# Kernel tuning notes

Measured on AMD Instinct MI355X. Metric: run time of the kernel, lower is better.

## Reference

```python
import jax, jax.numpy as jnp
import numpy as np

N_NODES = 10000
N_EDGES = 320000
N_GRAPHS = 64
L = 3  # num_layers


def _gru(a, h, wih, whh, bih, bhh):
    # torch.nn.GRUCell math: input a, hidden h
    gi = a @ wih.T + bih
    gh = h @ whh.T + bhh
    ir, iz, inn = jnp.split(gi, 3, axis=-1)
    hr, hz, hn = jnp.split(gh, 3, axis=-1)
    r = jax.nn.sigmoid(ir + hr)
    z = jax.nn.sigmoid(iz + hz)
    n = jnp.tanh(inn + r * hn)
    return (1.0 - z) * n + z * h


def _ggc(x, src, dst, w, wih, whh, bih, bhh):
    # PyG GatedGraphConv: pad features up to out_channels, then L rounds of
    # (linear -> scatter-add over edges -> GRUCell update)
    out_ch = w.shape[-1]
    if x.shape[-1] < out_ch:
        x = jnp.concatenate(
            [x, jnp.zeros((x.shape[0], out_ch - x.shape[-1]), x.dtype)], axis=-1)
    for i in range(w.shape[0]):
        m = x @ w[i]                                        # [N, C]
        a = jax.ops.segment_sum(m[src], dst, num_segments=N_NODES)  # scatter-add
        x = _gru(a, x, wih, whh, bih, bhh)
    return x


def setup_inputs() -> dict:
    key = jax.random.key(0)
    ks = jax.random.split(key, 16)
    d1, d2 = 128, 256
    s1, s2 = 1.0 / np.sqrt(d1), 1.0 / np.sqrt(d2)
    x = jax.random.normal(ks[0], (N_NODES, d1), dtype=jnp.float32)
    edge_index = jax.random.randint(ks[1], (2, N_EDGES), 0, N_NODES, dtype=jnp.int64)
    batch = jnp.sort(jax.random.randint(ks[2], (N_NODES,), 0, N_GRAPHS, dtype=jnp.int64))
    return {
        "x": x,
        "edge_index": edge_index,
        "batch": batch,
        "w1": jax.random.normal(ks[3], (L, d1, d1), jnp.float32) * s1,
        "gru1_wih": jax.random.normal(ks[4], (3 * d1, d1), jnp.float32) * s1,
        "gru1_whh": jax.random.normal(ks[5], (3 * d1, d1), jnp.float32) * s1,
        "gru1_bih": jax.random.normal(ks[6], (3 * d1,), jnp.float32) * s1,
        "gru1_bhh": jax.random.normal(ks[7], (3 * d1,), jnp.float32) * s1,
        "w2": jax.random.normal(ks[8], (L, d2, d2), jnp.float32) * s2,
        "gru2_wih": jax.random.normal(ks[9], (3 * d2, d2), jnp.float32) * s2,
        "gru2_whh": jax.random.normal(ks[10], (3 * d2, d2), jnp.float32) * s2,
        "gru2_bih": jax.random.normal(ks[11], (3 * d2,), jnp.float32) * s2,
        "gru2_bhh": jax.random.normal(ks[12], (3 * d2,), jnp.float32) * s2,
        "fc_w": jax.random.normal(ks[13], (6, d2), jnp.float32) * s2,
        "fc_b": jnp.zeros((6,), jnp.float32),
    }


def reference(x, edge_index, batch, w1, gru1_wih, gru1_whh, gru1_bih, gru1_bhh,
              w2, gru2_wih, gru2_whh, gru2_bih, gru2_bhh, fc_w, fc_b):
    src, dst = edge_index[0], edge_index[1]
    y = jax.nn.relu(_ggc(x, src, dst, w1, gru1_wih, gru1_whh, gru1_bih, gru1_bhh))
    y = _ggc(y, src, dst, w2, gru2_wih, gru2_whh, gru2_bih, gru2_bhh)
    y = jax.ops.segment_max(y, batch, num_segments=N_GRAPHS)  # global max pool [G, 256]
    return y @ fc_w.T + fc_b  # [G, 6]
```

## Files before the change

kernel.cpp:

```cpp
#include <hip/hip_runtime.h>

#define NN 10000
#define NNP 10112
#define NE 320000
#define NG 64
#define D1 128
#define D2 256
#define MT128 79

typedef unsigned short u16;
typedef short v8s __attribute__((ext_vector_type(8)));
typedef float v4f __attribute__((ext_vector_type(4)));

__device__ __forceinline__ u16 f2bf(float x) {
    unsigned u = __float_as_uint(x);
    return (u16)((u + 0x7fffu + ((u >> 16) & 1u)) >> 16);
}
__device__ __forceinline__ float bf2f(u16 b) {
    return __uint_as_float(((unsigned)b) << 16);
}
__device__ __forceinline__ float sigm(float x) { return 1.f / (1.f + __expf(-x)); }
__device__ __forceinline__ float tanh_f(float x) {
    float cx = fminf(fmaxf(x, -15.f), 15.f);
    float e = __expf(2.f * cx);
    return (e - 1.f) / (e + 1.f);
}

#define MF(d, a, b) d = __builtin_amdgcn_mfma_f32_16x16x32_bf16(a, b, d, 0, 0, 0)

#define GLDS16(gp, lp)                                                         \
    __builtin_amdgcn_global_load_lds(                                          \
        (__attribute__((address_space(1))) unsigned int*)(unsigned long long)(gp), \
        (__attribute__((address_space(3))) unsigned int*)(lp), 16, 0, 0)


template<int C, int MODE, int OS, int NPT>
__global__ __launch_bounds__(256, 3)
void giqru_k(const u16* __restrict__ Ah, const u16* __restrict__ Al,
             const u16* __restrict__ Xh, const u16* __restrict__ Xl,
             const u16* __restrict__ WcH, const u16* __restrict__ WcL,
             const float* __restrict__ bih, const float* __restrict__ bhh,
             u16* __restrict__ xh_out, u16* __restrict__ xl_out,
             float* __restrict__ xf_out,
             const int* __restrict__ batch, unsigned* __restrict__ pool) {
    const int bid = blockIdx.x;
    const int l_ = bid >> 3;
    const int byt = (bid & 7) * 10 + l_ % 10;
    const int px = l_ / 10;
    if (byt >= MT128) return;
    __shared__ u16 lds[16384];
    const int tid = threadIdx.x;
    const int wave = tid >> 6, lane = tid & 63;
    const int wr = wave >> 1, wc = wave & 1;
    const int quad = lane >> 4, r16 = lane & 15;
    const int bm = byt * 128;
    constexpr int K2 = 2 * C;
    constexpr int NK = K2 >> 5;
    constexpr int CCH = C >> 3;
    const size_t art = (size_t)(byt * 2);
    const size_t wrow = (size_t)px * (K2 >> 3);

    v4f acc[4][4] = {};
    u16 hsh[4][4], hsl[4][4];
    for (int ks = 0; ks < NK; ++ks) {
        const int k0 = ks << 5;
        const bool ap = k0 < C;
        const u16* sh = ap ? Ah : Xh;
        const u16* sl = ap ? Al : Xl;
        const int kc = (ap ? k0 : k0 - C) >> 3;
#pragma unroll
        for (int s2 = 0; s2 < 8; ++s2) {
            int u = s2 * 4 + wave;
            const u16* gp; int ld;
            if (u < 8)       { int t = u >> 2, q = u & 3;
                gp = sh + ((art + t) * CCH + kc + q) * 512;            ld = q * 1024 + t * 512; }
            else if (u < 16) { int v = u - 8; int t = v >> 2, q = v & 3;
                gp = sl + ((art + t) * CCH + kc + q) * 512;            ld = 4096 + q * 1024 + t * 512; }
            else if (u < 24) { int v = u - 16; int q = v >> 1, h = v & 1;
                gp = WcH + (wrow + (k0 >> 3) + q) * 1024 + h * 512;    ld = 8192 + q * 1024 + h * 512; }
            else             { int v = u - 24; int q = v >> 1, h = v & 1;
                gp = WcL + (wrow + (k0 >> 3) + q) * 1024 + h * 512;    ld = 12288 + q * 1024 + h * 512; }
            GLDS16(gp + lane * 8, &lds[ld]);
        }
        __syncthreads();
        if (!ap && (k0 - C) == px * 32) {
            const int kl = wc * 16 + r16;
            const int q = kl >> 3, kr = kl & 7;
#pragma unroll
            for (int i = 0; i < 4; ++i)
#pragma unroll
                for (int r = 0; r < 4; ++r) {
                    int lr = wr * 64 + i * 16 + quad * 4 + r;
                    int idx = q * 1024 + (lr >> 6) * 512 + (lr & 63) * 8 + kr;
                    hsh[i][r] = lds[idx];
                    hsl[i][r] = lds[4096 + idx];
                }
        }
        v8s fah[4], fal[4];
#pragma unroll
        for (int i = 0; i < 4; ++i) {
            int ra = (quad * 128 + wr * 64 + i * 16 + r16) * 8;
            fah[i] = *(const v8s*)&lds[ra];
            fal[i] = *(const v8s*)&lds[4096 + ra];
        }
        const int g2 = ap ? 2 : 3;
        const int p0 = 8192 + (quad * 128 + wc * 64 + r16) * 8;
        v8s w0h = *(const v8s*)&lds[p0];
        v8s w0l = *(const v8s*)&lds[4096 + p0];
        v8s w1h = *(const v8s*)&lds[p0 + 128];
        v8s w1l = *(const v8s*)&lds[4096 + p0 + 128];
        v8s w2h = *(const v8s*)&lds[p0 + g2 * 128];
        v8s w2l = *(const v8s*)&lds[4096 + p0 + g2 * 128];
#pragma unroll
        for (int i = 0; i < 4; ++i) {
            MF(acc[i][0], fah[i], w0h); MF(acc[i][0], fah[i], w0l); MF(acc[i][0], fal[i], w0h);
            MF(acc[i][1], fah[i], w1h); MF(acc[i][1], fah[i], w1l); MF(acc[i][1], fal[i], w1h);
            if (ap) {
                MF(acc[i][2], fah[i], w2h); MF(acc[i][2], fah[i], w2l); MF(acc[i][2], fal[i], w2h);
            } else {
                MF(acc[i][3], fah[i], w2h); MF(acc[i][3], fah[i], w2l); MF(acc[i][3], fal[i], w2h);
            }
        }
        __syncthreads();
    }

    const int c = px * 32 + wc * 16 + r16;
    const float br = bih[c] + bhh[c];
    const float bz = bih[C + c] + bhh[C + c];
    const float bi_n = bih[2 * C + c];
    const float bh_n = bhh[2 * C + c];
    const int cch = c >> 3, cr = c & 7;
#pragma unroll
    for (int i = 0; i < 4; ++i) {
        int R0 = bm + wr * 64 + i * 16 + quad * 4;
#pragma unroll
        for (int r = 0; r < 4; ++r) {
            int R = R0 + r;
            if (R >= NN) continue;
            float rr = sigm(acc[i][0][r] + br);
            float zz = sigm(acc[i][1][r] + bz);
            float nn_ = tanh_f(acc[i][2][r] + bi_n + rr * (acc[i][3][r] + bh_n));
            float h = bf2f(hsh[i][r]) + bf2f(hsl[i][r]);
            float o = (1.f - zz) * nn_ + zz * h;
            if (MODE == 2) {
                unsigned b = __float_as_uint(o);
                unsigned u = (b & 0x80000000u) ? ~b : (b | 0x80000000u);
                atomicMax(&pool[batch[R] * 256 + c], u);
            } else {
                if (MODE == 1) o = fmaxf(o, 0.f);
                size_t ox = ((size_t)(R >> 6) * (OS >> 3) + cch) * 512 + ((R & 63) << 3) + cr;
                u16 hh = f2bf(o);
                xh_out[ox] = hh;
                xl_out[ox] = f2bf(o - bf2f(hh));
                xf_out[(size_t)R * OS + c] = o;
            }
        }
    }
}

__global__ void count_k(const int* __restrict__ dst, int* __restrict__ cnt) {
    int e = blockIdx.x * blockDim.x + threadIdx.x;
    if (e < NE) atomicAdd(&cnt[dst[e]], 1);
}

__global__ void scan_k(const int* __restrict__ cnt, int* __restrict__ off,
                       int* __restrict__ cur) {
    __shared__ int ps[1024];
    const int tid = threadIdx.x;
    const int CH = (NN + 1023) / 1024;
    const int base = tid * CH;
    int s = 0;
    for (int i = 0; i < CH; ++i) {
        int idx = base + i;
        if (idx < NN) s += cnt[idx];
    }
    ps[tid] = s;
    __syncthreads();
    for (int d = 1; d < 1024; d <<= 1) {
        int v = (tid >= d) ? ps[tid - d] : 0;
        __syncthreads();
        ps[tid] += v;
        __syncthreads();
    }
    int run = (tid > 0) ? ps[tid - 1] : 0;
    for (int i = 0; i < CH; ++i) {
        int idx = base + i;
        if (idx <= NN) { off[idx] = run; if (idx < NN) cur[idx] = run; }
        if (idx < NN) run += cnt[idx];
    }
}

__global__ void fill_k(const int* __restrict__ src, const int* __restrict__ dst,
                       int* __restrict__ cur, int* __restrict__ elist) {
    int e = blockIdx.x * blockDim.x + threadIdx.x;
    if (e >= NE) return;
    int p = atomicAdd(&cur[dst[e]], 1);
    elist[p] = src[e];
}

template<int C>
__global__ void gather_k(const float* __restrict__ xf, const int* __restrict__ off,
                         const int* __restrict__ elist,
                         u16* __restrict__ ah, u16* __restrict__ al) {
    constexpr int LPN = C / 4;
    const int GB = gridDim.x;
    const int q = GB >> 3, r = GB & 7;
    const int xx = blockIdx.x & 7, oo = blockIdx.x >> 3;
    const int wg = (xx < r ? xx * (q + 1) : r * (q + 1) + (xx - r) * q) + oo;
    int t = wg * 256 + threadIdx.x;
    int node = t / LPN;
    if (node >= NN) return;
    int c = (t % LPN) * 4;
    int s0 = off[node], s1 = off[node + 1];
    v4f a0 = 0.f, a1 = 0.f, a2 = 0.f, a3 = 0.f;
    int i = s0;
    for (; i + 4 <= s1; i += 4) {
        int e0 = elist[i], e1 = elist[i + 1], e2 = elist[i + 2], e3 = elist[i + 3];
        v4f v0 = *(const v4f*)(xf + (size_t)e0 * C + c);
        v4f v1 = *(const v4f*)(xf + (size_t)e1 * C + c);
        v4f v2 = *(const v4f*)(xf + (size_t)e2 * C + c);
        v4f v3 = *(const v4f*)(xf + (size_t)e3 * C + c);
        a0 += v0; a1 += v1; a2 += v2; a3 += v3;
    }
    for (; i < s1; ++i) {
        int e = elist[i];
        a0 += *(const v4f*)(xf + (size_t)e * C + c);
    }
    v4f acc = (a0 + a1) + (a2 + a3);
    ushort4 h, l;
    h.x = f2bf(acc[0]); l.x = f2bf(acc[0] - bf2f(h.x));
    h.y = f2bf(acc[1]); l.y = f2bf(acc[1] - bf2f(h.y));
    h.z = f2bf(acc[2]); l.z = f2bf(acc[2] - bf2f(h.z));
    h.w = f2bf(acc[3]); l.w = f2bf(acc[3] - bf2f(h.w));
    size_t ox = ((size_t)(node >> 6) * (C >> 3) + (c >> 3)) * 512 + ((node & 63) << 3) + (c & 7);
    *(ushort4*)(ah + ox) = h;
    *(ushort4*)(al + ox) = l;
}

__global__ void weff_k(const float* __restrict__ w, const float* __restrict__ wih,
                       u16* __restrict__ WcH, u16* __restrict__ WcL, int C) {
    __shared__ float As[64 * 65];
    __shared__ float Bs[64 * 65];
    const int k0 = blockIdx.x * 64, jp0 = blockIdx.y * 64, it = blockIdx.z;
    const int tid = threadIdx.x;
    const int tx = tid & 15, ty = tid >> 4;
    const int K2 = 2 * C;
    float acc[4][4] = {};
    for (int j0 = 0; j0 < C; j0 += 64) {
        for (int idx = tid; idx < 4096; idx += 256) {
            int row = idx >> 6, j = idx & 63;
            As[row * 65 + j] = w[((size_t)it * C + k0 + row) * C + j0 + j];
            int jp = jp0 + row;
            int cc = ((jp >> 6) << 4) | (jp & 15);
            int g = (jp >> 4) & 3;
            Bs[row * 65 + j] = (g < 3) ? wih[((size_t)g * C + cc) * C + j0 + j] : 0.f;
        }
        __syncthreads();
        for (int j = 0; j < 64; ++j) {
            float a0 = As[(tx * 4 + 0) * 65 + j];
            float a1 = As[(tx * 4 + 1) * 65 + j];
            float a2 = As[(tx * 4 + 2) * 65 + j];
            float a3 = As[(tx * 4 + 3) * 65 + j];
            float b0 = Bs[(ty * 4 + 0) * 65 + j];
            float b1 = Bs[(ty * 4 + 1) * 65 + j];
            float b2 = Bs[(ty * 4 + 2) * 65 + j];
            float b3 = Bs[(ty * 4 + 3) * 65 + j];
            acc[0][0] += b0 * a0; acc[0][1] += b0 * a1; acc[0][2] += b0 * a2; acc[0][3] += b0 * a3;
            acc[1][0] += b1 * a0; acc[1][1] += b1 * a1; acc[1][2] += b1 * a2; acc[1][3] += b1 * a3;
            acc[2][0] += b2 * a0; acc[2][1] += b2 * a1; acc[2][2] += b2 * a2; acc[2][3] += b2 * a3;
            acc[3][0] += b3 * a0; acc[3][1] += b3 * a1; acc[3][2] += b3 * a2; acc[3][3] += b3 * a3;
        }
        __syncthreads();
    }
    const size_t its = (size_t)it * 8 * C * C;
#pragma unroll
    for (int a = 0; a < 4; ++a) {
        int jp = jp0 + ty * 4 + a;
#pragma unroll
        for (int b = 0; b < 4; ++b) {
            int k = k0 + tx * 4 + b;
            float v = acc[a][b];
            u16 h = f2bf(v);
            size_t o = its + ((size_t)(jp >> 7) * (K2 >> 3) + (k >> 3)) * 1024 + ((jp & 127) << 3) + (k & 7);
            WcH[o] = h;
            WcL[o] = f2bf(v - bf2f(h));
        }
    }
}

__global__ void prep_k(const float* __restrict__ whh1, const float* __restrict__ whh2,
                       const float* __restrict__ xin,
                       u16* __restrict__ Wc1h, u16* __restrict__ Wc1l,
                       u16* __restrict__ Wc2h, u16* __restrict__ Wc2l,
                       u16* __restrict__ xh, u16* __restrict__ xl) {
    const int q1 = 3 * 512 * 128;
    const int q2 = 3 * 1024 * 256;
    int t = blockIdx.x * blockDim.x + threadIdx.x;
    if (t < q1) {
        int it = t / (512 * 128), r = t - it * (512 * 128);
        int jp = r >> 7, kk = r & 127;
        int c = ((jp >> 6) << 4) | (jp & 15);
        int g = (jp >> 4) & 3;
        float v = (g == 0) ? whh1[c * D1 + kk]
                : (g == 1) ? whh1[(D1 + c) * D1 + kk]
                : (g == 2) ? 0.f
                           : whh1[(2 * D1 + c) * D1 + kk];
        int k = D1 + kk;
        u16 h = f2bf(v);
        size_t o = (size_t)it * 131072 + ((size_t)(jp >> 7) * 32 + (k >> 3)) * 1024 + ((jp & 127) << 3) + (k & 7);
        Wc1h[o] = h; Wc1l[o] = f2bf(v - bf2f(h)); return;
    }
    t -= q1;
    if (t < q2) {
        int it = t / (1024 * 256), r = t - it * (1024 * 256);
        int jp = r >> 8, kk = r & 255;
        int c = ((jp >> 6) << 4) | (jp & 15);
        int g = (jp >> 4) & 3;
        float v = (g == 0) ? whh2[c * D2 + kk]
                : (g == 1) ? whh2[(D2 + c) * D2 + kk]
                : (g == 2) ? 0.f
                           : whh2[(2 * D2 + c) * D2 + kk];
        int k = D2 + kk;
        u16 h = f2bf(v);
        size_t o = (size_t)it * 524288 + ((size_t)(jp >> 7) * 64 + (k >> 3)) * 1024 + ((jp & 127) << 3) + (k & 7);
        Wc2h[o] = h; Wc2l[o] = f2bf(v - bf2f(h)); return;
    }
    t -= q2;
    if (t < NN * D1) {
        int n = t >> 7, cc = t & 127;
        float v = xin[t];
        u16 h = f2bf(v);
        size_t o = ((size_t)(n >> 6) * 16 + (cc >> 3)) * 512 + ((n & 63) << 3) + (cc & 7);
        xh[o] = h;
        xl[o] = f2bf(v - bf2f(h));
    }
}

__global__ void pad_k(u16* __restrict__ xh, u16* __restrict__ xl,
                      float* __restrict__ xf) {
    int t = blockIdx.x * blockDim.x + threadIdx.x;
    if (t >= NNP * 128) return;
    int n = t >> 7, c = 128 + (t & 127);
    size_t o = ((size_t)(n >> 6) * 32 + (c >> 3)) * 512 + ((n & 63) << 3) + (c & 7);
    xh[o] = 0;
    xl[o] = 0;
    xf[(size_t)n * 256 + c] = 0.f;
}

__global__ void pool_init_k(unsigned* __restrict__ pool) {
    int t = blockIdx.x * blockDim.x + threadIdx.x;
    if (t < NG * D2) pool[t] = 0x007FFFFFu;
}

__global__ void fc_k(const unsigned* __restrict__ pool, const float* __restrict__ w,
                     const float* __restrict__ b, float* __restrict__ out) {
    int t = blockIdx.x * blockDim.x + threadIdx.x;
    if (t >= NG * 6) return;
    int g = t / 6, o = t - g * 6;
    float s = b[o];
    for (int c = 0; c < D2; ++c) {
        unsigned u = pool[g * D2 + c];
        unsigned bits = (u & 0x80000000u) ? (u ^ 0x80000000u) : ~u;
        s += __uint_as_float(bits) * w[o * D2 + c];
    }
    out[t] = s;
}

extern "C" void kernel_launch(void* const* d_in, const int* in_sizes, int n_in,
                              void* d_out, int out_size, void* d_ws, size_t ws_size,
                              hipStream_t stream) {
    const float* x_in = (const float*)d_in[0];
    const int* ei = (const int*)d_in[1];
    const int* src = ei;
    const int* dst = ei + NE;
    const int* batch = (const int*)d_in[2];
    const float* w1   = (const float*)d_in[3];
    const float* wih1 = (const float*)d_in[4];
    const float* whh1 = (const float*)d_in[5];
    const float* bih1 = (const float*)d_in[6];
    const float* bhh1 = (const float*)d_in[7];
    const float* w2   = (const float*)d_in[8];
    const float* wih2 = (const float*)d_in[9];
    const float* whh2 = (const float*)d_in[10];
    const float* bih2 = (const float*)d_in[11];
    const float* bhh2 = (const float*)d_in[12];
    const float* fcw  = (const float*)d_in[13];
    const float* fcb  = (const float*)d_in[14];
    float* out = (float*)d_out;

    u16* a_h  = (u16*)d_ws;
    u16* a_l  = a_h + (size_t)NNP * 256;
    u16* xA0h = a_l + (size_t)NNP * 256;
    u16* xA0l = xA0h + (size_t)NNP * 128;
    u16* xA1h = xA0l + (size_t)NNP * 128;
    u16* xA1l = xA1h + (size_t)NNP * 128;
    u16* xB0h = xA1l + (size_t)NNP * 128;
    u16* xB0l = xB0h + (size_t)NNP * 256;
    u16* xB1h = xB0l + (size_t)NNP * 256;
    u16* xB1l = xB1h + (size_t)NNP * 256;
    u16* Wc1h = xB1l + (size_t)NNP * 256;
    u16* Wc1l = Wc1h + (size_t)3 * 512 * 256;
    u16* Wc2h = Wc1l + (size_t)3 * 512 * 256;
    u16* Wc2l = Wc2h + (size_t)3 * 1024 * 512;
    float* xfA = (float*)(Wc2l + (size_t)3 * 1024 * 512);
    float* xfB = xfA + (size_t)NNP * 128;
    int* cnt   = (int*)(xfB + (size_t)NNP * 256);
    int* off   = cnt + NN;
    int* cur   = off + NN + 1;
    int* elist = cur + NN;
    unsigned* pool = (unsigned*)(elist + NE);

    hipMemsetAsync(cnt, 0, NN * sizeof(int), stream);
    count_k<<<(NE + 255) / 256, 256, 0, stream>>>(dst, cnt);
    scan_k<<<1, 1024, 0, stream>>>(cnt, off, cur);
    fill_k<<<(NE + 255) / 256, 256, 0, stream>>>(src, dst, cur, elist);
    {
        int total = 3 * 512 * 128 + 3 * 1024 * 256 + NN * D1;
        prep_k<<<(total + 255) / 256, 256, 0, stream>>>(
            whh1, whh2, x_in, Wc1h, Wc1l, Wc2h, Wc2l, xA0h, xA0l);
    }
    weff_k<<<dim3(D1 / 64, 4 * D1 / 64, 3), 256, 0, stream>>>(w1, wih1, Wc1h, Wc1l, D1);
    weff_k<<<dim3(D2 / 64, 4 * D2 / 64, 3), 256, 0, stream>>>(w2, wih2, Wc2h, Wc2l, D2);
    pad_k<<<(NNP * 128 + 255) / 256, 256, 0, stream>>>(xB0h, xB0l, xfB);
    pool_init_k<<<(NG * D2 + 255) / 256, 256, 0, stream>>>(pool);

    const int G1 = 8 * 10 * 4;
    const int G2 = 8 * 10 * 8;
    const int GG1 = (NN * (D1 / 4) + 255) / 256;
    const int GG2 = (NN * (D2 / 4) + 255) / 256;
    const size_t W1S = 131072, W2S = 524288;

    gather_k<D1><<<GG1, 256, 0, stream>>>(x_in, off, elist, a_h, a_l);
    giqru_k<D1, 0, 128, 4><<<G1, 256, 0, stream>>>(
        a_h, a_l, xA0h, xA0l, Wc1h, Wc1l, bih1, bhh1,
        xA1h, xA1l, xfA, nullptr, nullptr);

    gather_k<D1><<<GG1, 256, 0, stream>>>(xfA, off, elist, a_h, a_l);
    giqru_k<D1, 0, 128, 4><<<G1, 256, 0, stream>>>(
        a_h, a_l, xA1h, xA1l, Wc1h + W1S, Wc1l + W1S, bih1, bhh1,
        xA0h, xA0l, xfA, nullptr, nullptr);

    gather_k<D1><<<GG1, 256, 0, stream>>>(xfA, off, elist, a_h, a_l);
    giqru_k<D1, 1, 256, 4><<<G1, 256, 0, stream>>>(
        a_h, a_l, xA0h, xA0l, Wc1h + 2 * W1S, Wc1l + 2 * W1S, bih1, bhh1,
        xB0h, xB0l, xfB, nullptr, nullptr);

    gather_k<D2><<<GG2, 256, 0, stream>>>(xfB, off, elist, a_h, a_l);
    giqru_k<D2, 0, 256, 8><<<G2, 256, 0, stream>>>(
        a_h, a_l, xB0h, xB0l, Wc2h, Wc2l, bih2, bhh2,
        xB1h, xB1l, xfB, nullptr, nullptr);

    gather_k<D2><<<GG2, 256, 0, stream>>>(xfB, off, elist, a_h, a_l);
    giqru_k<D2, 0, 256, 8><<<G2, 256, 0, stream>>>(
        a_h, a_l, xB1h, xB1l, Wc2h + W2S, Wc2l + W2S, bih2, bhh2,
        xB0h, xB0l, xfB, nullptr, nullptr);

    gather_k<D2><<<GG2, 256, 0, stream>>>(xfB, off, elist, a_h, a_l);
    giqru_k<D2, 2, 256, 8><<<G2, 256, 0, stream>>>(
        a_h, a_l, xB0h, xB0l, Wc2h + 2 * W2S, Wc2l + 2 * W2S, bih2, bhh2,
        nullptr, nullptr, nullptr, batch, pool);

    fc_k<<<1, 512, 0, stream>>>(pool, fcw, fcb, out);
}
```

Baseline: 583.5 us.

## Partition edge gather by source-node chunk to improve cache locality

Edges are bucketed by destination node and by one of four source-node ranges, and each gather becomes four passes, one per source range. Partial sums accumulate in an fp32 buffer, and the last pass converts them to the split-bf16 tiled layout. Each pass touches a smaller slice of the feature table so gathers should hit in L2 more often. The cost is four launches per gather, extra read/write traffic for partial sums, and shorter per-pass edge loops with less memory parallelism.

```diff
diff --git a/kernel.cpp b/kernel.cpp
--- a/kernel.cpp
+++ b/kernel.cpp
@@ -7,6 +7,8 @@
 #define D1 128
 #define D2 256
 #define MT128 79
+#define NCH 4
+#define CHS 2500
 
 typedef unsigned short u16;
 typedef short v8s __attribute__((ext_vector_type(8)));
@@ -158,21 +160,23 @@
     }
 }
 
-__global__ void count_k(const int* __restrict__ dst, int* __restrict__ cnt) {
+__global__ void count_k(const int* __restrict__ src, const int* __restrict__ dst,
+                        int* __restrict__ cnt) {
     int e = blockIdx.x * blockDim.x + threadIdx.x;
-    if (e < NE) atomicAdd(&cnt[dst[e]], 1);
+    if (e < NE) atomicAdd(&cnt[dst[e] * NCH + src[e] / CHS], 1);
 }
 
 __global__ void scan_k(const int* __restrict__ cnt, int* __restrict__ off,
                        int* __restrict__ cur) {
     __shared__ int ps[1024];
     const int tid = threadIdx.x;
-    const int CH = (NN + 1023) / 1024;
+    const int TOT = NN * NCH;
+    const int CH = (TOT + 1023) / 1024;
     const int base = tid * CH;
     int s = 0;
     for (int i = 0; i < CH; ++i) {
         int idx = base + i;
-        if (idx < NN) s += cnt[idx];
+        if (idx < TOT) s += cnt[idx];
     }
     ps[tid] = s;
     __syncthreads();
@@ -185,8 +189,8 @@
     int run = (tid > 0) ? ps[tid - 1] : 0;
     for (int i = 0; i < CH; ++i) {
         int idx = base + i;
-        if (idx <= NN) { off[idx] = run; if (idx < NN) cur[idx] = run; }
-        if (idx < NN) run += cnt[idx];
+        if (idx <= TOT) { off[idx] = run; if (idx < TOT) cur[idx] = run; }
+        if (idx < TOT) run += cnt[idx];
     }
 }
 
@@ -194,14 +198,14 @@
                        int* __restrict__ cur, int* __restrict__ elist) {
     int e = blockIdx.x * blockDim.x + threadIdx.x;
     if (e >= NE) return;
-    int p = atomicAdd(&cur[dst[e]], 1);
+    int p = atomicAdd(&cur[dst[e] * NCH + src[e] / CHS], 1);
     elist[p] = src[e];
 }
 
-template<int C>
-__global__ void gather_k(const float* __restrict__ xf, const int* __restrict__ off,
-                         const int* __restrict__ elist,
-                         u16* __restrict__ ah, u16* __restrict__ al) {
+template<int C, int GM>
+__global__ void gatherp_k(const float* __restrict__ xf, const int* __restrict__ off,
+                          const int* __restrict__ elist, float* __restrict__ part,
+                          u16* __restrict__ ah, u16* __restrict__ al, int ph) {
     constexpr int LPN = C / 4;
     const int GB = gridDim.x;
     const int q = GB >> 3, r = GB & 7;
@@ -211,30 +215,34 @@
     int node = t / LPN;
     if (node >= NN) return;
     int c = (t % LPN) * 4;
-    int s0 = off[node], s1 = off[node + 1];
+    int s0 = off[node * NCH + ph], s1 = off[node * NCH + ph + 1];
     v4f a0 = 0.f, a1 = 0.f, a2 = 0.f, a3 = 0.f;
     int i = s0;
     for (; i + 4 <= s1; i += 4) {
         int e0 = elist[i], e1 = elist[i + 1], e2 = elist[i + 2], e3 = elist[i + 3];
-        v4f v0 = *(const v4f*)(xf + (size_t)e0 * C + c);
-        v4f v1 = *(const v4f*)(xf + (size_t)e1 * C + c);
-        v4f v2 = *(const v4f*)(xf + (size_t)e2 * C + c);
-        v4f v3 = *(const v4f*)(xf + (size_t)e3 * C + c);
-        a0 += v0; a1 += v1; a2 += v2; a3 += v3;
+        a0 += *(const v4f*)(xf + (size_t)e0 * C + c);
+        a1 += *(const v4f*)(xf + (size_t)e1 * C + c);
+        a2 += *(const v4f*)(xf + (size_t)e2 * C + c);
+        a3 += *(const v4f*)(xf + (size_t)e3 * C + c);
     }
     for (; i < s1; ++i) {
         int e = elist[i];
         a0 += *(const v4f*)(xf + (size_t)e * C + c);
     }
     v4f acc = (a0 + a1) + (a2 + a3);
-    ushort4 h, l;
-    h.x = f2bf(acc[0]); l.x = f2bf(acc[0] - bf2f(h.x));
-    h.y = f2bf(acc[1]); l.y = f2bf(acc[1] - bf2f(h.y));
-    h.z = f2bf(acc[2]); l.z = f2bf(acc[2] - bf2f(h.z));
-    h.w = f2bf(acc[3]); l.w = f2bf(acc[3] - bf2f(h.w));
-    size_t ox = ((size_t)(node >> 6) * (C >> 3) + (c >> 3)) * 512 + ((node & 63) << 3) + (c & 7);
-    *(ushort4*)(ah + ox) = h;
-    *(ushort4*)(al + ox) = l;
+    if (GM != 0) acc += *(const v4f*)(part + (size_t)node * C + c);
+    if (GM == 2) {
+        ushort4 h, l;
+        h.x = f2bf(acc[0]); l.x = f2bf(acc[0] - bf2f(h.x));
+        h.y = f2bf(acc[1]); l.y = f2bf(acc[1] - bf2f(h.y));
+        h.z = f2bf(acc[2]); l.z = f2bf(acc[2] - bf2f(h.z));
+        h.w = f2bf(acc[3]); l.w = f2bf(acc[3] - bf2f(h.w));
+        size_t ox = ((size_t)(node >> 6) * (C >> 3) + (c >> 3)) * 512 + ((node & 63) << 3) + (c & 7);
+        *(ushort4*)(ah + ox) = h;
+        *(ushort4*)(al + ox) = l;
+    } else {
+        *(v4f*)(part + (size_t)node * C + c) = acc;
+    }
 }
 
 __global__ void weff_k(const float* __restrict__ w, const float* __restrict__ wih,
@@ -404,14 +412,15 @@
     u16* Wc2l = Wc2h + (size_t)3 * 1024 * 512;
     float* xfA = (float*)(Wc2l + (size_t)3 * 1024 * 512);
     float* xfB = xfA + (size_t)NNP * 128;
-    int* cnt   = (int*)(xfB + (size_t)NNP * 256);
-    int* off   = cnt + NN;
-    int* cur   = off + NN + 1;
-    int* elist = cur + NN;
+    float* pbuf = xfB + (size_t)NNP * 256;
+    int* cnt   = (int*)(pbuf + (size_t)NNP * 256);
+    int* off   = cnt + NN * NCH;
+    int* cur   = off + NN * NCH + 1;
+    int* elist = cur + NN * NCH;
     unsigned* pool = (unsigned*)(elist + NE);
 
-    hipMemsetAsync(cnt, 0, NN * sizeof(int), stream);
-    count_k<<<(NE + 255) / 256, 256, 0, stream>>>(dst, cnt);
+    hipMemsetAsync(cnt, 0, NN * NCH * sizeof(int), stream);
+    count_k<<<(NE + 255) / 256, 256, 0, stream>>>(src, dst, cnt);
     scan_k<<<1, 1024, 0, stream>>>(cnt, off, cur);
     fill_k<<<(NE + 255) / 256, 256, 0, stream>>>(src, dst, cur, elist);
     {
@@ -430,32 +439,40 @@
     const int GG2 = (NN * (D2 / 4) + 255) / 256;
     const size_t W1S = 131072, W2S = 524288;
 
-    gather_k<D1><<<GG1, 256, 0, stream>>>(x_in, off, elist, a_h, a_l);
+#define GATHER(CC, GRID, XF)                                                       \
+    do {                                                                           \
+        gatherp_k<CC, 0><<<GRID, 256, 0, stream>>>(XF, off, elist, pbuf, a_h, a_l, 0); \
+        gatherp_k<CC, 1><<<GRID, 256, 0, stream>>>(XF, off, elist, pbuf, a_h, a_l, 1); \
+        gatherp_k<CC, 1><<<GRID, 256, 0, stream>>>(XF, off, elist, pbuf, a_h, a_l, 2); \
+        gatherp_k<CC, 2><<<GRID, 256, 0, stream>>>(XF, off, elist, pbuf, a_h, a_l, 3); \
+    } while (0)
+
+    GATHER(D1, GG1, x_in);
     giqru_k<D1, 0, 128, 4><<<G1, 256, 0, stream>>>(
         a_h, a_l, xA0h, xA0l, Wc1h, Wc1l, bih1, bhh1,
         xA1h, xA1l, xfA, nullptr, nullptr);
 
-    gather_k<D1><<<GG1, 256, 0, stream>>>(xfA, off, elist, a_h, a_l);
+    GATHER(D1, GG1, xfA);
     giqru_k<D1, 0, 128, 4><<<G1, 256, 0, stream>>>(
         a_h, a_l, xA1h, xA1l, Wc1h + W1S, Wc1l + W1S, bih1, bhh1,
         xA0h, xA0l, xfA, nullptr, nullptr);
 
-    gather_k<D1><<<GG1, 256, 0, stream>>>(xfA, off, elist, a_h, a_l);
+    GATHER(D1, GG1, xfA);
     giqru_k<D1, 1, 256, 4><<<G1, 256, 0, stream>>>(
         a_h, a_l, xA0h, xA0l, Wc1h + 2 * W1S, Wc1l + 2 * W1S, bih1, bhh1,
         xB0h, xB0l, xfB, nullptr, nullptr);
 
-    gather_k<D2><<<GG2, 256, 0, stream>>>(xfB, off, elist, a_h, a_l);
+    GATHER(D2, GG2, xfB);
     giqru_k<D2, 0, 256, 8><<<G2, 256, 0, stream>>>(
         a_h, a_l, xB0h, xB0l, Wc2h, Wc2l, bih2, bhh2,
         xB1h, xB1l, xfB, nullptr, nullptr);
 
-    gather_k<D2><<<GG2, 256, 0, stream>>>(xfB, off, elist, a_h, a_l);
+    GATHER(D2, GG2, xfB);
     giqru_k<D2, 0, 256, 8><<<G2, 256, 0, stream>>>(
         a_h, a_l, xB1h, xB1l, Wc2h + W2S, Wc2l + W2S, bih2, bhh2,
         xB0h, xB0l, xfB, nullptr, nullptr);
 
-    gather_k<D2><<<GG2, 256, 0, stream>>>(xfB, off, elist, a_h, a_l);
+    GATHER(D2, GG2, xfB);
     giqru_k<D2, 2, 256, 8><<<G2, 256, 0, stream>>>(
         a_h, a_l, xB0h, xB0l, Wc2h + 2 * W2S, Wc2l + 2 * W2S, bih2, bhh2,
         nullptr, nullptr, nullptr, batch, pool);
```

Result: slower. 709.5 us (+21.6%).
